# Optimization experiments

Measured on AMD Instinct MI355X. Metric: run time of the kernel, lower is better.

## Reference

```python
import jax, jax.numpy as jnp
import numpy as np

DIM = 1024
N_HEADS = 8
N_KV_HEADS = 8
Q_C = 128
Q_NOPE = 96
Q_ROPE = 32
KV_C = 128
K_NOPE = 64
K_ROPE = 64
V_HD = 256
EPS = 1e-8
ROPE_THETA = 10000.0


def rms_norm(x, w, eps=EPS):
    return w * x * jax.lax.rsqrt(jnp.mean(x * x, axis=-1, keepdims=True) + eps)


def apply_rope(x, position_ids, head_dim):
    # x: [B, H, S, hd], interleaved even/odd rotation (matches torch module)
    inv_freq = 1.0 / (ROPE_THETA ** (jnp.arange(0, head_dim, 2, dtype=jnp.float32) / head_dim))
    ang = position_ids.astype(jnp.float32)[:, None, :, None] * inv_freq  # [B,1,S,hd/2]
    cos, sin = jnp.cos(ang), jnp.sin(ang)
    xe, xo = x[..., ::2], x[..., 1::2]
    rot = jnp.stack((xe * cos - xo * sin, xe * sin + xo * cos), axis=-1)
    return rot.reshape(x.shape)


def setup_inputs() -> dict:
    key = jax.random.key(0)
    ks = jax.random.split(key, 12)
    B, S = 2, 2048
    s = 0.02
    return {
        "x": jax.random.normal(ks[0], (B, S, DIM), jnp.float32),
        "position_ids": jnp.broadcast_to(jnp.arange(S, dtype=jnp.int32), (B, S)),
        "w_dq_w": jax.random.normal(ks[1], (DIM, Q_C), jnp.float32) * s,
        "w_dq_b": jnp.zeros((Q_C,), jnp.float32),
        "q_norm_w": jnp.ones((Q_C,), jnp.float32),
        "w_uq_qr_w": jax.random.normal(ks[2], (Q_C, N_HEADS * (Q_NOPE + Q_ROPE)), jnp.float32) * s,
        "w_uq_qr_b": jnp.zeros((N_HEADS * (Q_NOPE + Q_ROPE),), jnp.float32),
        "w_dkv_kr_w": jax.random.normal(ks[3], (DIM, KV_C + K_ROPE), jnp.float32) * s,
        "w_dkv_kr_b": jnp.zeros((KV_C + K_ROPE,), jnp.float32),
        "kv_norm_w": jnp.ones((KV_C,), jnp.float32),
        "w_uk_uv_w": jax.random.normal(ks[4], (KV_C, N_KV_HEADS * (K_NOPE + V_HD)), jnp.float32) * s,
        "w_uk_uv_b": jnp.zeros((N_KV_HEADS * (K_NOPE + V_HD),), jnp.float32),
        "w_o_w": jax.random.normal(ks[5], (N_HEADS * V_HD, DIM), jnp.float32) * s,
        "w_o_b": jnp.zeros((DIM,), jnp.float32),
    }


def reference(x, position_ids, w_dq_w, w_dq_b, q_norm_w, w_uq_qr_w, w_uq_qr_b,
              w_dkv_kr_w, w_dkv_kr_b, kv_norm_w, w_uk_uv_w, w_uk_uv_b, w_o_w, w_o_b):
    B, S, _ = x.shape
    # --- Q path: compress -> norm -> up-project, split nope/rope ---
    cq = rms_norm(x @ w_dq_w + w_dq_b, q_norm_w)                     # [B,S,Qc]
    q = cq @ w_uq_qr_w + w_uq_qr_b                                   # [B,S,H*(96+32)]
    q_nope, q_rope = jnp.split(q, [N_HEADS * Q_NOPE], axis=-1)
    q_nope = q_nope.reshape(B, S, N_HEADS, Q_NOPE).transpose(0, 2, 1, 3)
    q_rope = q_rope.reshape(B, S, N_HEADS, Q_ROPE).transpose(0, 2, 1, 3)
    q_rope = apply_rope(q_rope, position_ids, Q_ROPE)
    q_states = jnp.concatenate((q_nope, q_rope), axis=-1)            # [B,H,S,128]
    # --- KV path: compress + shared rope key ---
    ckv_kr = x @ w_dkv_kr_w + w_dkv_kr_b
    ckv, k_rope = jnp.split(ckv_kr, [KV_C], axis=-1)
    ckv = rms_norm(ckv, kv_norm_w)                                   # [B,S,KVc]
    k_rope = apply_rope(k_rope[:, None, :, :], position_ids, K_ROPE) # [B,1,S,64]
    kv = ckv @ w_uk_uv_w + w_uk_uv_b                                 # [B,S,KVh*(64+256)]
    k_nope, v = jnp.split(kv, [N_KV_HEADS * K_NOPE], axis=-1)
    k_nope = k_nope.reshape(B, S, N_KV_HEADS, K_NOPE).transpose(0, 2, 1, 3)
    k_rope = jnp.broadcast_to(k_rope, (B, N_KV_HEADS, S, K_ROPE))
    k_states = jnp.concatenate((k_nope, k_rope), axis=-1)            # [B,KVh,S,128]
    v_states = v.reshape(B, S, N_KV_HEADS, V_HD).transpose(0, 2, 1, 3)
    # gqa_factor = n_heads // n_kv_heads = 1 -> repeat is a no-op
    # --- SDPA (no mask), scale = 1/sqrt(q head dim) ---
    scale = 1.0 / jnp.sqrt(jnp.float32(Q_NOPE + Q_ROPE))
    scores = jnp.einsum("bhqd,bhkd->bhqk", q_states, k_states) * scale
    probs = jax.nn.softmax(scores, axis=-1)
    attn = jnp.einsum("bhqk,bhkd->bhqd", probs, v_states)            # [B,H,S,256]
    attn = attn.transpose(0, 2, 1, 3).reshape(B, S, N_HEADS * V_HD)
    return attn @ w_o_w + w_o_b
```

## Files before the change

### kernel.cpp

```cpp
#include <hip/hip_runtime.h>
#include <hip/hip_bf16.h>
#include <stdint.h>

typedef unsigned short u16;
typedef short short8 __attribute__((ext_vector_type(8)));
typedef float floatx4 __attribute__((ext_vector_type(4)));

#define S_LEN 2048
#define NB 2
#define NH 8
#define R_TOK (NB * S_LEN)

#define L2_THETA 13.287712379549449f
#define QSCALE (0.08838834764831845f * 1.4426950408889634f)

__device__ inline u16 f2bf(float f) {
  union { float f; uint32_t u; } x; x.f = f;
  uint32_t r = (x.u + 0x7fffu + ((x.u >> 16) & 1u)) >> 16;
  return (u16)r;
}
__device__ inline float bf2f(u16 h) {
  union { uint32_t u; float f; } x; x.u = ((uint32_t)h) << 16;
  return x.f;
}
__device__ inline floatx4 mfma16(short8 a, short8 b, floatx4 c) {
  return __builtin_amdgcn_mfma_f32_16x16x32_bf16(a, b, c, 0, 0, 0);
}
__device__ inline uint32_t pkbf(float a, float b) {
  union { __hip_bfloat162 h; uint32_t u; } c;
  c.h = __float22bfloat162_rn(make_float2(a, b));
  return c.u;
}
__device__ __forceinline__ void cp16(const void* g, const void* l) {
  __builtin_amdgcn_global_load_lds(
      (const __attribute__((address_space(1))) uint32_t*)(uintptr_t)g,
      (__attribute__((address_space(3))) uint32_t*)(uintptr_t)l, 16, 0, 0);
}

__global__ __launch_bounds__(256) void k_prep(
    const float* __restrict__ x, u16* __restrict__ xbf,
    const float* __restrict__ wdq, const float* __restrict__ wdkv, u16* __restrict__ waT,
    const float* __restrict__ wuq, u16* __restrict__ wQT,
    const float* __restrict__ wukv, u16* __restrict__ wKVT,
    const float* __restrict__ wo, u16* __restrict__ wOT,
    const float* __restrict__ bdq, const float* __restrict__ bdkv,
    float* __restrict__ biasA) {
  __shared__ u16 tile[32][33];
  const int s = blockIdx.x, tid = threadIdx.x;
  const int tx = tid & 31, ty = tid >> 5;
  if (s < 4096) {
    int i = s * 256 + tid;
    float4 v = ((const float4*)x)[i];
    ushort4 o;
    o.x = f2bf(v.x); o.y = f2bf(v.y); o.z = f2bf(v.z); o.w = f2bf(v.w);
    ((ushort4*)xbf)[i] = o;
  } else if (s < 4416) {
    int t = s - 4096, bx = t % 10, by = t / 10;
    int c0 = bx * 32, r0 = by * 32;
#pragma unroll
    for (int i = 0; i < 4; ++i) {
      int r = r0 + ty + i * 8, c = c0 + tx;
      float v = (c < 128) ? wdq[(size_t)r * 128 + c] : wdkv[(size_t)r * 192 + (c - 128)];
      tile[ty + i * 8][tx] = f2bf(v);
    }
    __syncthreads();
#pragma unroll
    for (int i = 0; i < 4; ++i)
      waT[(size_t)(c0 + ty + i * 8) * 1024 + r0 + tx] = tile[tx][ty + i * 8];
  } else {
    const float* in; u16* out; int R, C, bx, by;
    if (s < 4544) { int t = s - 4416; in = wuq; out = wQT; R = 128; C = 1024; bx = t & 31; by = t >> 5; }
    else if (s < 4864) { int t = s - 4544; in = wukv; out = wKVT; R = 128; C = 2560; bx = t % 80; by = t / 80; }
    else if (s < 6912) { int t = s - 4864; in = wo; out = wOT; R = 2048; C = 1024; bx = t & 31; by = t >> 5; }
    else {
      if (tid < 320) biasA[tid] = (tid < 128) ? bdq[tid] : bdkv[tid - 128];
      return;
    }
    int c0 = bx * 32, r0 = by * 32;
#pragma unroll
    for (int i = 0; i < 4; ++i)
      tile[ty + i * 8][tx] = f2bf(in[(size_t)(r0 + ty + i * 8) * C + c0 + tx]);
    __syncthreads();
#pragma unroll
    for (int i = 0; i < 4; ++i)
      out[(size_t)(c0 + ty + i * 8) * R + r0 + tx] = tile[tx][ty + i * 8];
  }
}

template <int OUT_BF>
__global__ __launch_bounds__(256) void k_gemm_bt(const u16* __restrict__ A,
                                                 const u16* __restrict__ BT,
                                                 const float* __restrict__ bias,
                                                 void* __restrict__ Cout,
                                                 int M, int N, int K) {
  __shared__ __align__(16) u16 Alds[2][128 * 32];
  __shared__ __align__(16) u16 Blds[2][128 * 32];
  const int tid = threadIdx.x;
  const int wave = tid >> 6, lane = tid & 63;
  const int lane15 = lane & 15, quad = lane >> 4;
  const int m0 = blockIdx.y * 128, n0 = blockIdx.x * 128;
  const int mw = (wave & 1) * 64, nw = (wave >> 1) * 64;

  floatx4 acc[4][4];
#pragma unroll
  for (int a = 0; a < 4; ++a)
#pragma unroll
    for (int b = 0; b < 4; ++b) acc[a][b] = (floatx4){0.f, 0.f, 0.f, 0.f};

  const int srow = wave * 32 + (lane >> 2);
  const int scol = (lane & 3) * 8;

  auto stage = [&](int k0, int buf) {
    const u16* ga = A + (size_t)(m0 + srow) * K + k0 + scol;
    cp16(ga, Alds[buf] + srow * 32 + scol);
    cp16(ga + (size_t)16 * K, Alds[buf] + (srow + 16) * 32 + scol);
    const u16* gb = BT + (size_t)(n0 + srow) * K + k0 + scol;
    cp16(gb, Blds[buf] + srow * 32 + scol);
    cp16(gb + (size_t)16 * K, Blds[buf] + (srow + 16) * 32 + scol);
  };

  stage(0, 0);
  int cur = 0;
  for (int k0 = 0; k0 < K; k0 += 32) {
    __syncthreads();
    if (k0 + 32 < K) stage(k0 + 32, cur ^ 1);
    short8 af[4], bf[4];
#pragma unroll
    for (int im = 0; im < 4; ++im)
      af[im] = *(const short8*)&Alds[cur][(mw + im * 16 + lane15) * 32 + quad * 8];
#pragma unroll
    for (int in = 0; in < 4; ++in)
      bf[in] = *(const short8*)&Blds[cur][(nw + in * 16 + lane15) * 32 + quad * 8];
#pragma unroll
    for (int im = 0; im < 4; ++im)
#pragma unroll
      for (int in = 0; in < 4; ++in) acc[im][in] = mfma16(af[im], bf[in], acc[im][in]);
    cur ^= 1;
  }

#pragma unroll
  for (int im = 0; im < 4; ++im)
#pragma unroll
    for (int in = 0; in < 4; ++in)
#pragma unroll
      for (int r = 0; r < 4; ++r) {
        int row = m0 + mw + im * 16 + quad * 4 + r;
        int col = n0 + nw + in * 16 + lane15;
        if (col < N) {
          float v = acc[im][in][r] + bias[col];
          if (OUT_BF)
            ((u16*)Cout)[(size_t)row * N + col] = f2bf(v);
          else
            ((float*)Cout)[(size_t)row * N + col] = v;
        }
      }
}

__global__ __launch_bounds__(256) void k_gemm_qkv(
    const u16* __restrict__ Aq, const u16* __restrict__ BTq,
    const float* __restrict__ biasq, const float* __restrict__ qtab,
    u16* __restrict__ qstates,
    const u16* __restrict__ Akv, const u16* __restrict__ BTkv,
    const float* __restrict__ biaskv, u16* __restrict__ kvb, u16* __restrict__ vT) {
  const int K = 128;
  __shared__ __align__(16) u16 Alds[2][128 * 32];
  __shared__ __align__(16) u16 Blds[2][128 * 32];
  __shared__ __align__(16) u16 eplds[64 * 136];
  const int tid = threadIdx.x;
  const int wave = tid >> 6, lane = tid & 63;
  const int lane15 = lane & 15, quad = lane >> 4;
  const bool isq = blockIdx.x < 256;
  int m0, n0;
  const u16 *A, *BT;
  if (isq) {
    int qb = blockIdx.x;
    m0 = (qb & 31) * 128;
    n0 = (qb >> 5) * 128;
    A = Aq; BT = BTq;
  } else {
    int kb = blockIdx.x - 256;
    n0 = (kb % 20) * 128;
    m0 = (kb / 20) * 128;
    A = Akv; BT = BTkv;
  }
  const int mw = (wave & 1) * 64, nw = (wave >> 1) * 64;

  floatx4 acc[4][4];
#pragma unroll
  for (int a = 0; a < 4; ++a)
#pragma unroll
    for (int b = 0; b < 4; ++b) acc[a][b] = (floatx4){0.f, 0.f, 0.f, 0.f};

  const int srow = wave * 32 + (lane >> 2);
  const int scol = (lane & 3) * 8;
  auto stage = [&](int k0, int buf) {
    const u16* ga = A + (size_t)(m0 + srow) * K + k0 + scol;
    cp16(ga, Alds[buf] + srow * 32 + scol);
    cp16(ga + (size_t)16 * K, Alds[buf] + (srow + 16) * 32 + scol);
    const u16* gb = BT + (size_t)(n0 + srow) * K + k0 + scol;
    cp16(gb, Blds[buf] + srow * 32 + scol);
    cp16(gb + (size_t)16 * K, Blds[buf] + (srow + 16) * 32 + scol);
  };

  stage(0, 0);
  int cur = 0;
  for (int k0 = 0; k0 < K; k0 += 32) {
    __syncthreads();
    if (k0 + 32 < K) stage(k0 + 32, cur ^ 1);
    short8 af[4], bf[4];
#pragma unroll
    for (int im = 0; im < 4; ++im)
      af[im] = *(const short8*)&Alds[cur][(mw + im * 16 + lane15) * 32 + quad * 8];
#pragma unroll
    for (int in = 0; in < 4; ++in)
      bf[in] = *(const short8*)&Blds[cur][(nw + in * 16 + lane15) * 32 + quad * 8];
#pragma unroll
    for (int im = 0; im < 4; ++im)
#pragma unroll
      for (int in = 0; in < 4; ++in) acc[im][in] = mfma16(af[im], bf[in], acc[im][in]);
    cur ^= 1;
  }

  if (isq) {
    const bool ropeblk = (n0 >= 768);
#pragma unroll
    for (int in = 0; in < 4; ++in) {
      const int col = n0 + nw + in * 16 + lane15;
#pragma unroll
      for (int im = 0; im < 4; ++im) {
        if (!ropeblk) {
          const int h = col / 96, d = col - h * 96;
#pragma unroll
          for (int r = 0; r < 4; ++r) {
            int row = m0 + mw + im * 16 + quad * 4 + r;
            int b = row >> 11, s = row & (S_LEN - 1);
            float v = acc[im][in][r] + biasq[col];
            qstates[((size_t)(b * NH + h) * S_LEN + s) * 128 + d] = f2bf(v * QSCALE);
          }
        } else {
          const int j = (col - 768) & 31, h = (col - 768) >> 5, pr = j >> 1;
#pragma unroll
          for (int r = 0; r < 4; ++r) {
            int row = m0 + mw + im * 16 + quad * 4 + r;
            int b = row >> 11, s = row & (S_LEN - 1);
            float v = acc[im][in][r] + biasq[col];
            float vp = __shfl_xor(v, 1);
            float xe = (lane & 1) ? vp : v;
            float xo = (lane & 1) ? v : vp;
            float2 cs = *(const float2*)&qtab[((size_t)row * 16 + pr) * 2];
            float val = (j & 1) ? (xe * cs.y + xo * cs.x) : (xe * cs.x - xo * cs.y);
            qstates[((size_t)(b * NH + h) * S_LEN + s) * 128 + 96 + j] = f2bf(val * QSCALE);
          }
        }
      }
    }
  } else if (n0 < 512) {
#pragma unroll
    for (int im = 0; im < 4; ++im)
#pragma unroll
      for (int in = 0; in < 4; ++in)
#pragma unroll
        for (int r = 0; r < 4; ++r) {
          int row = m0 + mw + im * 16 + quad * 4 + r;
          int col = n0 + nw + in * 16 + lane15;
          kvb[(size_t)row * 2560 + col] = f2bf(acc[im][in][r] + biaskv[col]);
        }
  } else {
    const int sbase = m0 & (S_LEN - 1), bq = m0 >> 11;
#pragma unroll
    for (int hh = 0; hh < 2; ++hh) {
#pragma unroll
      for (int im = 0; im < 4; ++im) {
        const int rrel = mw + im * 16 + quad * 4;
        const int bb = (rrel & 63) >> 2;
        const int a = (bb & 8) | (((bb >> 1) & 1) << 2) | ((bb & 1) << 1) | ((bb >> 2) & 1);
        const int prel = (rrel >> 6) * 64 + a * 4;
#pragma unroll
        for (int ii = 0; ii < 2; ++ii) {
          const int in = hh * 2 + ii;
          const int nl = nw + in * 16 + lane15;
          const int slot = (nl & 31) | ((nl & 64) >> 1);
          const float bv = biaskv[n0 + nl];
          ushort4 o;
          o.x = f2bf(acc[im][in][0] + bv);
          o.y = f2bf(acc[im][in][1] + bv);
          o.z = f2bf(acc[im][in][2] + bv);
          o.w = f2bf(acc[im][in][3] + bv);
          *(ushort4*)&eplds[slot * 136 + prel] = o;
        }
      }
      __syncthreads();
#pragma unroll
      for (int i = 0; i < 4; ++i) {
        int idx = i * 256 + tid;
        int slot = idx >> 4, c8 = (idx & 15) * 8;
        int nl = (slot & 31) + hh * 32 + ((slot & 32) << 1);
        int c2 = n0 + nl - 512;
        int hv = c2 >> 8, nn = c2 & 255;
        short8 v = *(const short8*)&eplds[slot * 136 + c8];
        *(short8*)&vT[((size_t)((bq * NH + hv) * 256 + nn)) * 2048 + sbase + c8] = v;
      }
      if (hh == 0) __syncthreads();
    }
  }
}

__global__ void k_stagea(const float* __restrict__ t0, const float* __restrict__ qnw,
                         const float* __restrict__ kvnw, const int* __restrict__ pos_ids,
                         u16* __restrict__ cq, u16* __restrict__ ckv,
                         u16* __restrict__ krope, float* __restrict__ qtab) {
  int r = blockIdx.x, tid = threadIdx.x;
  const float* row = t0 + (size_t)r * 320;
  float a = row[tid];
  float b = row[128 + tid];
  float sa = a * a, sb = b * b;
#pragma unroll
  for (int d = 1; d < 64; d <<= 1) {
    sa += __shfl_xor(sa, d);
    sb += __shfl_xor(sb, d);
  }
  __shared__ float red[4];
  if ((tid & 63) == 0) { red[(tid >> 6) * 2] = sa; red[(tid >> 6) * 2 + 1] = sb; }
  __syncthreads();
  sa = red[0] + red[2];
  sb = red[1] + red[3];
  float ra = rsqrtf(sa * (1.0f / 128.0f) + 1e-8f);
  float rb = rsqrtf(sb * (1.0f / 128.0f) + 1e-8f);
  cq[(size_t)r * 128 + tid] = f2bf(qnw[tid] * a * ra);
  ckv[(size_t)r * 128 + tid] = f2bf(kvnw[tid] * b * rb);
  if (tid < 32) {
    float xe = row[256 + 2 * tid], xo = row[256 + 2 * tid + 1];
    float p = (float)pos_ids[r];
    float freq = exp2f(-(2.0f * tid / 64.0f) * L2_THETA);
    float ang = p * freq;
    float c = cosf(ang), s = sinf(ang);
    krope[(size_t)r * 64 + 2 * tid] = f2bf(xe * c - xo * s);
    krope[(size_t)r * 64 + 2 * tid + 1] = f2bf(xe * s + xo * c);
  } else if (tid < 48) {
    int pr = tid - 32;
    float p = (float)pos_ids[r];
    float freq = exp2f(-(2.0f * pr / 32.0f) * L2_THETA);
    float ang = p * freq;
    qtab[((size_t)r * 16 + pr) * 2] = cosf(ang);
    qtab[((size_t)r * 16 + pr) * 2 + 1] = sinf(ang);
  }
}

__global__ __launch_bounds__(512) void k_attn(const u16* __restrict__ qstates,
                                              const u16* __restrict__ kv,
                                              const u16* __restrict__ krope,
                                              const u16* __restrict__ vT,
                                              u16* __restrict__ attn_out) {
  const int pair = blockIdx.x;
  const int qblk = blockIdx.y;
  const int b = pair >> 3, h = pair & 7;
  const int tid = threadIdx.x;
  const int wave = tid >> 6, lane = tid & 63;
  const int lane15 = lane & 15, quad = lane >> 4;
  const int w4 = wave & 3, half = wave >> 2;

  __shared__ __align__(16) u16 Klds[2][64 * 128];
  __shared__ __align__(16) u16 Vlds[2][256 * 64];

  const int qrow0 = qblk * 128 + wave * 16;
  short8 qfrag[4];
  {
    const u16* qb = qstates + ((size_t)(b * NH + h) * S_LEN + qrow0 + lane15) * 128 + quad * 8;
#pragma unroll
    for (int c = 0; c < 4; ++c) qfrag[c] = *(const short8*)(qb + c * 32);
  }

  floatx4 o_acc[16];
#pragma unroll
  for (int g = 0; g < 16; ++g) o_acc[g] = (floatx4){0.f, 0.f, 0.f, 0.f};
  float m_i = -1e30f;
  float l_i = 0.f;

  const int kbase = (quad * 16 + lane15) * 8;
  int vo0[4], vo1[4];
#pragma unroll
  for (int ph = 0; ph < 4; ++ph) {
    int n = ph * 16 + lane15;
    int sw = (n ^ (n >> 3)) & 7;
    vo0[ph] = n * 64 + ((quad ^ sw) & 7) * 8;
    vo1[ph] = n * 64 + (((quad | 4) ^ sw) & 7) * 8;
  }

  const u16* kp[2];
  int kstr[2];
  int kdst[2];
#pragma unroll
  for (int j = 0; j < 2; ++j) {
    int u = half * 8 + j * 4 + quad;
    const u16* base;
    int str;
    if (u < 8) { base = kv + h * 64 + u * 8; str = 2560; }
    else { base = krope + (u - 8) * 8; str = 64; }
    kp[j] = base + (size_t)(b * S_LEN + w4 * 16 + lane15) * str;
    kstr[j] = str;
    kdst[j] = (w4 * 256 + (half * 2 + j) * 64 + lane) * 8;
  }
  const int vn6 = tid >> 3, vsl = tid & 7;
  const u16* vp[4];
#pragma unroll
  for (int oi = 0; oi < 4; ++oi) {
    int n = oi * 64 + vn6;
    int u = vsl ^ ((n ^ (n >> 3)) & 7);
    vp[oi] = vT + ((size_t)pair * 256 + n) * 2048 + u * 8;
  }

  auto issueK = [&](int buf) {
#pragma unroll
    for (int j = 0; j < 2; ++j) {
      cp16(kp[j], &Klds[buf][kdst[j]]);
      kp[j] += (size_t)64 * kstr[j];
    }
  };
  auto issueV = [&](int buf) {
#pragma unroll
    for (int oi = 0; oi < 4; ++oi) {
      cp16(vp[oi], &Vlds[buf][(oi * 512 + tid) * 8]);
      vp[oi] += 64;
    }
  };

  issueK(0);
  issueV(0);
  asm volatile("s_waitcnt vmcnt(0)" ::: "memory");
  __builtin_amdgcn_sched_barrier(0);
  __builtin_amdgcn_s_barrier();

  int cur = 0;
  for (int ch = 0; ch < S_LEN / 64; ++ch) {
    if (ch + 1 < S_LEN / 64) {
      issueK(cur ^ 1);
      issueV(cur ^ 1);
    }

    floatx4 st[4];
#pragma unroll
    for (int t = 0; t < 4; ++t) st[t] = (floatx4){0.f, 0.f, 0.f, 0.f};
    __builtin_amdgcn_s_setprio(1);
#pragma unroll
    for (int c = 0; c < 4; ++c) {
      short8 qf = qfrag[c];
#pragma unroll
      for (int t = 0; t < 4; ++t) {
        short8 kf = *(const short8*)&Klds[cur][kbase + (t * 16 + c * 4) * 128];
        st[t] = mfma16(kf, qf, st[t]);
      }
    }
    __builtin_amdgcn_s_setprio(0);

    float mloc = st[0][0];
#pragma unroll
    for (int t = 0; t < 4; ++t)
#pragma unroll
      for (int r = 0; r < 4; ++r) mloc = fmaxf(mloc, st[t][r]);
    mloc = fmaxf(mloc, __shfl_xor(mloc, 16));
    mloc = fmaxf(mloc, __shfl_xor(mloc, 32));

    const bool resc = __any(mloc > m_i + 8.0f);
    const float mref = resc ? fmaxf(m_i, mloc) : m_i;

    float rs = 0.f;
    union { short8 s; uint4 u; } a01, a23;
    {
      float p0, p1, p2, p3;
      p0 = exp2f(st[0][0] - mref); p1 = exp2f(st[0][1] - mref);
      p2 = exp2f(st[0][2] - mref); p3 = exp2f(st[0][3] - mref);
      rs += (p0 + p1) + (p2 + p3);
      a01.u.x = pkbf(p0, p1); a01.u.y = pkbf(p2, p3);
      p0 = exp2f(st[1][0] - mref); p1 = exp2f(st[1][1] - mref);
      p2 = exp2f(st[1][2] - mref); p3 = exp2f(st[1][3] - mref);
      rs += (p0 + p1) + (p2 + p3);
      a01.u.z = pkbf(p0, p1); a01.u.w = pkbf(p2, p3);
      p0 = exp2f(st[2][0] - mref); p1 = exp2f(st[2][1] - mref);
      p2 = exp2f(st[2][2] - mref); p3 = exp2f(st[2][3] - mref);
      rs += (p0 + p1) + (p2 + p3);
      a23.u.x = pkbf(p0, p1); a23.u.y = pkbf(p2, p3);
      p0 = exp2f(st[3][0] - mref); p1 = exp2f(st[3][1] - mref);
      p2 = exp2f(st[3][2] - mref); p3 = exp2f(st[3][3] - mref);
      rs += (p0 + p1) + (p2 + p3);
      a23.u.z = pkbf(p0, p1); a23.u.w = pkbf(p2, p3);
    }

    if (resc) {
      float alpha = exp2f(m_i - mref);
      m_i = mref;
      l_i = l_i * alpha + rs;
      float al[4];
#pragma unroll
      for (int r = 0; r < 4; ++r) al[r] = __shfl(alpha, quad * 4 + r, 16);
#pragma unroll
      for (int g = 0; g < 16; ++g) {
        o_acc[g][0] *= al[0]; o_acc[g][1] *= al[1];
        o_acc[g][2] *= al[2]; o_acc[g][3] *= al[3];
      }
    } else {
      l_i += rs;
    }

    __builtin_amdgcn_s_setprio(1);
#pragma unroll
    for (int g = 0; g < 16; ++g) {
      short8 b01 = *(const short8*)&Vlds[cur][vo0[g & 3] + (g >> 2) * 4096];
      short8 b23 = *(const short8*)&Vlds[cur][vo1[g & 3] + (g >> 2) * 4096];
      floatx4 o = o_acc[g];
      o = mfma16(a01.s, b01, o);
      o = mfma16(a23.s, b23, o);
      o_acc[g] = o;
    }
    __builtin_amdgcn_s_setprio(0);

    asm volatile("s_waitcnt vmcnt(0)" ::: "memory");
    __builtin_amdgcn_sched_barrier(0);
    __builtin_amdgcn_s_barrier();
    cur ^= 1;
  }

  float lsum = l_i;
  lsum += __shfl_xor(lsum, 16);
  lsum += __shfl_xor(lsum, 32);
  float rl = 1.0f / lsum;
  float linv[4];
#pragma unroll
  for (int r = 0; r < 4; ++r) linv[r] = __shfl(rl, quad * 4 + r, 16);
#pragma unroll
  for (int g = 0; g < 16; ++g) {
#pragma unroll
    for (int r = 0; r < 4; ++r) {
      int row = qrow0 + quad * 4 + r;
      int col = h * 256 + g * 16 + lane15;
      attn_out[((size_t)b * S_LEN + row) * 2048 + col] = f2bf(o_acc[g][r] * linv[r]);
    }
  }
}

extern "C" void kernel_launch(void* const* d_in, const int* in_sizes, int n_in,
                              void* d_out, int out_size, void* d_ws, size_t ws_size,
                              hipStream_t stream) {
  const float* x = (const float*)d_in[0];
  const int* pos = (const int*)d_in[1];
  const float* wdq = (const float*)d_in[2];
  const float* bdq = (const float*)d_in[3];
  const float* qnw = (const float*)d_in[4];
  const float* wuq = (const float*)d_in[5];
  const float* buq = (const float*)d_in[6];
  const float* wdkv = (const float*)d_in[7];
  const float* bdkv = (const float*)d_in[8];
  const float* kvnw = (const float*)d_in[9];
  const float* wukv = (const float*)d_in[10];
  const float* bukv = (const float*)d_in[11];
  const float* wo = (const float*)d_in[12];
  const float* bo = (const float*)d_in[13];
  float* out = (float*)d_out;

  char* ws = (char*)d_ws;
  size_t off = 0;
  auto alloc = [&](size_t bytes) {
    char* p = ws + off;
    off += (bytes + 255) & ~(size_t)255;
    return p;
  };
  u16* xbf = (u16*)alloc((size_t)R_TOK * 1024 * 2);
  float* t0 = (float*)alloc((size_t)R_TOK * 320 * 4);
  u16* qout = (u16*)alloc((size_t)R_TOK * 1024 * 2);
  u16* vT = (u16*)d_ws;
  u16* waT = (u16*)alloc((size_t)384 * 1024 * 2);
  float* biasA = (float*)alloc(320 * 4);
  u16* wQT = (u16*)alloc((size_t)1024 * 128 * 2);
  u16* wKVT = (u16*)alloc((size_t)2560 * 128 * 2);
  u16* wOT = (u16*)alloc((size_t)1024 * 2048 * 2);
  u16* cq = (u16*)alloc((size_t)R_TOK * 128 * 2);
  u16* ckv = (u16*)alloc((size_t)R_TOK * 128 * 2);
  u16* krope = (u16*)alloc((size_t)R_TOK * 64 * 2);
  u16* qst = (u16*)alloc((size_t)R_TOK * 1024 * 2);
  u16* kvb = (u16*)alloc((size_t)R_TOK * 2560 * 2);
  u16* attnb = (u16*)alloc((size_t)R_TOK * 2048 * 2);
  float* qtab = (float*)alloc((size_t)R_TOK * 16 * 2 * 4);
  (void)ws_size; (void)n_in; (void)in_sizes; (void)out_size; (void)qout;

  k_prep<<<6913, 256, 0, stream>>>(x, xbf, wdq, wdkv, waT, wuq, wQT, wukv, wKVT, wo, wOT,
                                   bdq, bdkv, biasA);

  k_gemm_bt<0><<<dim3(3, 32), 256, 0, stream>>>(xbf, waT, biasA, t0, R_TOK, 320, 1024);
  k_stagea<<<R_TOK, 128, 0, stream>>>(t0, qnw, kvnw, pos, cq, ckv, krope, qtab);
  k_gemm_qkv<<<896, 256, 0, stream>>>(cq, wQT, buq, qtab, qst, ckv, wKVT, bukv, kvb, vT);
  k_attn<<<dim3(16, 16), 512, 0, stream>>>(qst, kvb, krope, vT, attnb);
  k_gemm_bt<0><<<dim3(8, 32), 256, 0, stream>>>(attnb, wOT, bo, out, R_TOK, 1024, 2048);
}
```

Before: 253.5 us.

## Overlap later weight transposes with the first projection GEMM in one launch

The prep kernel is split so that only the x conversion, the first-stage weight transpose and the bias packing run before the first GEMM. The remaining weight transposes (wuq, wukv, wo) move into extra blocks of a combined kernel that also runs the 4096x320 projection GEMM. Those blocks fill CUs that the 96-block GEMM grid would otherwise leave idle, and one launch is removed. The cost is a heavier kernel with shared-memory allocation for both roles, which may affect occupancy.

```diff
diff --git a/kernel.cpp b/kernel.cpp
--- a/kernel.cpp
+++ b/kernel.cpp
@@ -37,12 +37,9 @@
       (__attribute__((address_space(3))) uint32_t*)(uintptr_t)l, 16, 0, 0);
 }
 
-__global__ __launch_bounds__(256) void k_prep(
+__global__ __launch_bounds__(256) void k_prep1(
     const float* __restrict__ x, u16* __restrict__ xbf,
     const float* __restrict__ wdq, const float* __restrict__ wdkv, u16* __restrict__ waT,
-    const float* __restrict__ wuq, u16* __restrict__ wQT,
-    const float* __restrict__ wukv, u16* __restrict__ wKVT,
-    const float* __restrict__ wo, u16* __restrict__ wOT,
     const float* __restrict__ bdq, const float* __restrict__ bdkv,
     float* __restrict__ biasA) {
   __shared__ u16 tile[32][33];
@@ -68,14 +65,25 @@
     for (int i = 0; i < 4; ++i)
       waT[(size_t)(c0 + ty + i * 8) * 1024 + r0 + tx] = tile[tx][ty + i * 8];
   } else {
+    if (tid < 320) biasA[tid] = (tid < 128) ? bdq[tid] : bdkv[tid - 128];
+  }
+}
+
+__global__ __launch_bounds__(256) void k_gemma_wt(
+    const u16* __restrict__ A, const u16* __restrict__ BT,
+    const float* __restrict__ bias, float* __restrict__ Cout,
+    const float* __restrict__ wuq, u16* __restrict__ wQT,
+    const float* __restrict__ wukv, u16* __restrict__ wKVT,
+    const float* __restrict__ wo, u16* __restrict__ wOT) {
+  const int tid = threadIdx.x;
+  if (blockIdx.x >= 96) {
+    __shared__ u16 tile[32][33];
+    int t = blockIdx.x - 96;
     const float* in; u16* out; int R, C, bx, by;
-    if (s < 4544) { int t = s - 4416; in = wuq; out = wQT; R = 128; C = 1024; bx = t & 31; by = t >> 5; }
-    else if (s < 4864) { int t = s - 4544; in = wukv; out = wKVT; R = 128; C = 2560; bx = t % 80; by = t / 80; }
-    else if (s < 6912) { int t = s - 4864; in = wo; out = wOT; R = 2048; C = 1024; bx = t & 31; by = t >> 5; }
-    else {
-      if (tid < 320) biasA[tid] = (tid < 128) ? bdq[tid] : bdkv[tid - 128];
-      return;
-    }
+    if (t < 128) { in = wuq; out = wQT; R = 128; C = 1024; bx = t & 31; by = t >> 5; }
+    else if (t < 448) { int u = t - 128; in = wukv; out = wKVT; R = 128; C = 2560; bx = u % 80; by = u / 80; }
+    else { int u = t - 448; in = wo; out = wOT; R = 2048; C = 1024; bx = u & 31; by = u >> 5; }
+    const int tx = tid & 31, ty = tid >> 5;
     int c0 = bx * 32, r0 = by * 32;
 #pragma unroll
     for (int i = 0; i < 4; ++i)
@@ -84,7 +92,62 @@
 #pragma unroll
     for (int i = 0; i < 4; ++i)
       out[(size_t)(c0 + ty + i * 8) * R + r0 + tx] = tile[tx][ty + i * 8];
-  }
+    return;
+  }
+  const int N = 320, K = 1024;
+  __shared__ __align__(16) u16 Alds[2][128 * 32];
+  __shared__ __align__(16) u16 Blds[2][128 * 32];
+  const int wave = tid >> 6, lane = tid & 63;
+  const int lane15 = lane & 15, quad = lane >> 4;
+  const int n0 = (blockIdx.x % 3) * 128, m0 = (blockIdx.x / 3) * 128;
+  const int mw = (wave & 1) * 64, nw = (wave >> 1) * 64;
+
+  floatx4 acc[4][4];
+#pragma unroll
+  for (int a = 0; a < 4; ++a)
+#pragma unroll
+    for (int b = 0; b < 4; ++b) acc[a][b] = (floatx4){0.f, 0.f, 0.f, 0.f};
+
+  const int srow = wave * 32 + (lane >> 2);
+  const int scol = (lane & 3) * 8;
+  auto stage = [&](int k0, int buf) {
+    const u16* ga = A + (size_t)(m0 + srow) * K + k0 + scol;
+    cp16(ga, Alds[buf] + srow * 32 + scol);
+    cp16(ga + (size_t)16 * K, Alds[buf] + (srow + 16) * 32 + scol);
+    const u16* gb = BT + (size_t)(n0 + srow) * K + k0 + scol;
+    cp16(gb, Blds[buf] + srow * 32 + scol);
+    cp16(gb + (size_t)16 * K, Blds[buf] + (srow + 16) * 32 + scol);
+  };
+
+  stage(0, 0);
+  int cur = 0;
+  for (int k0 = 0; k0 < K; k0 += 32) {
+    __syncthreads();
+    if (k0 + 32 < K) stage(k0 + 32, cur ^ 1);
+    short8 af[4], bf[4];
+#pragma unroll
+    for (int im = 0; im < 4; ++im)
+      af[im] = *(const short8*)&Alds[cur][(mw + im * 16 + lane15) * 32 + quad * 8];
+#pragma unroll
+    for (int in = 0; in < 4; ++in)
+      bf[in] = *(const short8*)&Blds[cur][(nw + in * 16 + lane15) * 32 + quad * 8];
+#pragma unroll
+    for (int im = 0; im < 4; ++im)
+#pragma unroll
+      for (int in = 0; in < 4; ++in) acc[im][in] = mfma16(af[im], bf[in], acc[im][in]);
+    cur ^= 1;
+  }
+
+#pragma unroll
+  for (int im = 0; im < 4; ++im)
+#pragma unroll
+    for (int in = 0; in < 4; ++in)
+#pragma unroll
+      for (int r = 0; r < 4; ++r) {
+        int row = m0 + mw + im * 16 + quad * 4 + r;
+        int col = n0 + nw + in * 16 + lane15;
+        if (col < N) Cout[(size_t)row * N + col] = acc[im][in][r] + bias[col];
+      }
 }
 
 template <int OUT_BF>
@@ -581,10 +644,9 @@
   float* qtab = (float*)alloc((size_t)R_TOK * 16 * 2 * 4);
   (void)ws_size; (void)n_in; (void)in_sizes; (void)out_size; (void)qout;
 
-  k_prep<<<6913, 256, 0, stream>>>(x, xbf, wdq, wdkv, waT, wuq, wQT, wukv, wKVT, wo, wOT,
-                                   bdq, bdkv, biasA);
-
-  k_gemm_bt<0><<<dim3(3, 32), 256, 0, stream>>>(xbf, waT, biasA, t0, R_TOK, 320, 1024);
+  k_prep1<<<4417, 256, 0, stream>>>(x, xbf, wdq, wdkv, waT, bdq, bdkv, biasA);
+  k_gemma_wt<<<2592, 256, 0, stream>>>(xbf, waT, biasA, t0,
+                                       wuq, wQT, wukv, wKVT, wo, wOT);
   k_stagea<<<R_TOK, 128, 0, stream>>>(t0, qnw, kvnw, pos, cq, ckv, krope, qtab);
   k_gemm_qkv<<<896, 256, 0, stream>>>(cq, wQT, buq, qtab, qst, ckv, wKVT, bukv, kvb, vT);
   k_attn<<<dim3(16, 16), 512, 0, stream>>>(qst, kvb, krope, vT, attnb);
```

Result: no change. 249.0 us, median of 2 (-1.8%).
